# Optimization experiments

Hardware: AMD Instinct MI355X
Metric: run time of the kernel (lower is better)

Reference implementation:

```python
import jax, jax.numpy as jnp
import numpy as np

STRICT_MAXIMA_BONUS = 10.0  # init kwarg strict_maxima_bonus


def _pad_rep(x):
    # replicate-pad spatial dims (D,H,W) by 1, matching kornia F.pad(..., 'replicate')
    return jnp.pad(x, ((0, 0), (0, 0), (1, 1), (1, 1), (1, 1)), mode='edge')


def _grad1(x):
    # kornia spatial_gradient3d(order=1, mode='diff'): central differences /2
    p = _pad_rep(x)
    c, l, r = slice(1, -1), slice(0, -2), slice(2, None)
    dx = 0.5 * (p[..., c, c, r] - p[..., c, c, l])  # d/dx along W
    dy = 0.5 * (p[..., c, r, c] - p[..., c, l, c])  # d/dy along H
    ds = 0.5 * (p[..., r, c, c] - p[..., l, c, c])  # d/ds along D
    return jnp.stack([dx, dy, ds], axis=-1)  # (B,C,D,H,W,3)


def _grad2(x):
    # kornia spatial_gradient3d(order=2, mode='diff'): channel order dxx,dyy,dss,dxy,dys,dxs
    p = _pad_rep(x)
    c, l, r = slice(1, -1), slice(0, -2), slice(2, None)
    dxx = p[..., c, c, l] + p[..., c, c, r] - 2.0 * x
    dyy = p[..., c, l, c] + p[..., c, r, c] - 2.0 * x
    dss = p[..., l, c, c] + p[..., r, c, c] - 2.0 * x
    dxy = p[..., c, l, l] + p[..., c, r, r] - p[..., c, r, l] - p[..., c, l, r]
    dys = p[..., l, l, c] + p[..., r, r, c] - p[..., r, l, c] - p[..., l, r, c]
    dxs = p[..., l, c, l] + p[..., r, c, r] - p[..., r, c, l] - p[..., l, c, r]
    return dxx, dyy, dss, dxy, dys, dxs


def _nms3d_mask(x):
    # kornia nms3d: x == maxpool3d(x, 3, stride 1, pad 1) (pad value -inf)
    mx = jax.lax.reduce_window(x, -jnp.inf, jax.lax.max,
                               (1, 1, 3, 3, 3), (1, 1, 1, 1, 1),
                               [(0, 0), (0, 0), (1, 1), (1, 1), (1, 1)])
    return x == mx


def _forward(x):
    B, C, D, H, W = x.shape
    b = _grad1(x)  # (B,C,D,H,W,3) order [dx,dy,ds]
    dxx, dyy, dss, dxy, dys, dxs = _grad2(x)
    dxy, dys, dxs = 0.25 * dxy, 0.25 * dys, 0.25 * dxs
    Hes = jnp.stack([dxx, dxy, dxs,
                     dxy, dyy, dys,
                     dxs, dys, dss], axis=-1).reshape(B, C, D, H, W, 3, 3)
    nms = _nms3d_mask(x)  # (B,C,D,H,W) bool
    # safe_solve_with_mask: LU solve valid where factorization succeeded (non-singular)
    det = jnp.linalg.det(Hes)
    solved = det != 0.0
    eye3 = jnp.eye(3, dtype=x.dtype)
    safe_H = jnp.where(solved[..., None, None], Hes, eye3)
    sol = jnp.linalg.solve(safe_H, b[..., None])[..., 0]  # (B,C,D,H,W,3)
    new_nms = nms & solved  # nms_mask.masked_scatter(nms_mask, solved_correctly)
    x_solved = jnp.where(new_nms[..., None], sol, 0.0)
    dx = -x_solved
    # zero refinements with any |component| > 0.7
    big = jnp.max(jnp.abs(dx), axis=-1, keepdims=True) > 0.7
    dx = jnp.where(big, 0.0, dx)
    dy_val = 0.5 * jnp.sum(b * dx, axis=-1)  # 0.5 * b^T dx per voxel
    y_max = x + dy_val + STRICT_MAXIMA_BONUS * new_nms.astype(x.dtype)
    # dx.flip(1): component order [s,y,x]; then move comps to axis 2 -> (B,C,3,D,H,W)
    dx_res = jnp.moveaxis(dx[..., ::-1], -1, 2)
    # kornia create_meshgrid3d(...).permute(0,4,1,2,3): channel values (d, w, h)
    dd, hh, ww = jnp.meshgrid(jnp.arange(D), jnp.arange(H), jnp.arange(W), indexing='ij')
    grid = jnp.stack([dd, ww, hh], axis=0).astype(x.dtype)  # (3,D,H,W)
    coords_max = grid[None, None] + dx_res  # (B,C,3,D,H,W)
    return coords_max, y_max


def setup_inputs() -> dict:
    key = jax.random.key(0)
    x = jax.random.normal(key, (2, 1, 8, 512, 512), dtype=jnp.float32)
    return {"x": x}


def reference(x):
    return _forward(x)
```

## Files before the change

kernel.cpp:

```cpp
#include <hip/hip_runtime.h>

namespace {

constexpr int Dd = 8, Hh = 512, Ww = 512, Bb = 2;
constexpr int PLANE = Hh * Ww;
constexpr size_t COORDS_SZ = (size_t)Bb * 3 * Dd * PLANE;

__global__ __launch_bounds__(256) void cqi_kernel(const float* __restrict__ x,
                                                  float* __restrict__ out) {
    const int tx = threadIdx.x;
    const int ty = threadIdx.y;
    const int w0 = tx << 2;
    const int h  = (blockIdx.y << 1) + ty;
    const int bd = blockIdx.z;
    const int b  = bd >> 3;
    const int d  = bd & 7;

    const float* pls[3];
    pls[0] = x + (size_t)(d > 0      ? bd - 1 : bd) * PLANE;
    pls[1] = x + (size_t)bd * PLANE;
    pls[2] = x + (size_t)(d < Dd - 1 ? bd + 1 : bd) * PLANE;

    const int rws[3] = { (h > 0      ? h - 1 : 0)      * Ww,
                          h * Ww,
                         (h < Hh - 1 ? h + 1 : h)      * Ww };

    const int wm = (w0 > 0)        ? w0 - 1 : 0;
    const int wp = (w0 + 4 < Ww)   ? w0 + 4 : Ww - 1;

    float r[3][3][6];
#pragma unroll
    for (int a = 0; a < 3; ++a) {
#pragma unroll
        for (int e = 0; e < 3; ++e) {
            const float* p = pls[a] + rws[e];
            const float4 q = *reinterpret_cast<const float4*>(p + w0);
            r[a][e][0] = p[wm];
            r[a][e][1] = q.x; r[a][e][2] = q.y; r[a][e][3] = q.z; r[a][e][4] = q.w;
            r[a][e][5] = p[wp];
        }
    }

    float oc0[4], oc1[4], oc2[4], oy[4];
#pragma unroll
    for (int i = 0; i < 4; ++i) {
        float v[3][3][3];
#pragma unroll
        for (int a = 0; a < 3; ++a)
#pragma unroll
            for (int e = 0; e < 3; ++e)
#pragma unroll
                for (int cc = 0; cc < 3; ++cc)
                    v[a][e][cc] = r[a][e][i + cc];

        const float c0 = v[1][1][1];

        const float fx = 0.5f * (v[1][1][2] - v[1][1][0]);
        const float fy = 0.5f * (v[1][2][1] - v[1][0][1]);
        const float fs = 0.5f * (v[2][1][1] - v[0][1][1]);

        const float dxx = v[1][1][0] + v[1][1][2] - 2.0f * c0;
        const float dyy = v[1][0][1] + v[1][2][1] - 2.0f * c0;
        const float dss = v[0][1][1] + v[2][1][1] - 2.0f * c0;
        const float dxy = 0.25f * (v[1][0][0] + v[1][2][2] - v[1][2][0] - v[1][0][2]);
        const float dys = 0.25f * (v[0][0][1] + v[2][2][1] - v[2][0][1] - v[0][2][1]);
        const float dxs = 0.25f * (v[0][1][0] + v[2][1][2] - v[2][1][0] - v[0][1][2]);

        float mx = v[0][0][0];
#pragma unroll
        for (int a = 0; a < 3; ++a)
#pragma unroll
            for (int e = 0; e < 3; ++e)
#pragma unroll
                for (int cc = 0; cc < 3; ++cc)
                    mx = fmaxf(mx, v[a][e][cc]);
        const bool nms = (c0 == mx);

        const float det = dxx * dyy * dss + dxy * dys * dxs + dxs * dxy * dys
                        - dxs * dyy * dxs - dxx * dys * dys - dxy * dxy * dss;
        const bool solved = (det != 0.0f);

        const float A00 = dyy * dss - dys * dys;
        const float A01 = dys * dxs - dxy * dss;
        const float A02 = dxy * dys - dyy * dxs;
        const float A11 = dxx * dss - dxs * dxs;
        const float A12 = dxy * dxs - dxx * dys;
        const float A22 = dxx * dyy - dxy * dxy;
        const float inv = 1.0f / det;
        const float sx = (A00 * fx + A01 * fy + A02 * fs) * inv;
        const float sy = (A01 * fx + A11 * fy + A12 * fs) * inv;
        const float ss = (A02 * fx + A12 * fy + A22 * fs) * inv;

        const bool newnms = nms && solved;
        float dxv = newnms ? -sx : 0.0f;
        float dyv = newnms ? -sy : 0.0f;
        float dsv = newnms ? -ss : 0.0f;

        const float mabs = fmaxf(fabsf(dxv), fmaxf(fabsf(dyv), fabsf(dsv)));
        const bool keep = (mabs <= 0.7f);
        dxv = keep ? dxv : 0.0f;
        dyv = keep ? dyv : 0.0f;
        dsv = keep ? dsv : 0.0f;

        const float dyval = 0.5f * (fx * dxv + fy * dyv + fs * dsv);

        oy[i]  = c0 + dyval + (newnms ? 10.0f : 0.0f);
        oc0[i] = (float)d + dsv;
        oc1[i] = (float)(w0 + i) + dyv;
        oc2[i] = (float)h + dxv;
    }

    float* coords = out;
    float* ymax   = out + COORDS_SZ;
    const size_t idx = (size_t)(h * Ww) + w0;
    const size_t cb  = ((size_t)(b * 3) * Dd + d) * PLANE + idx;
    *reinterpret_cast<float4*>(coords + cb)                          = make_float4(oc0[0], oc0[1], oc0[2], oc0[3]);
    *reinterpret_cast<float4*>(coords + cb + (size_t)Dd * PLANE)     = make_float4(oc1[0], oc1[1], oc1[2], oc1[3]);
    *reinterpret_cast<float4*>(coords + cb + (size_t)2 * Dd * PLANE) = make_float4(oc2[0], oc2[1], oc2[2], oc2[3]);
    *reinterpret_cast<float4*>(ymax + (size_t)bd * PLANE + idx)      = make_float4(oy[0], oy[1], oy[2], oy[3]);
}

}

extern "C" void kernel_launch(void* const* d_in, const int* in_sizes, int n_in,
                              void* d_out, int out_size, void* d_ws, size_t ws_size,
                              hipStream_t stream) {
    const float* x = (const float*)d_in[0];
    float* out = (float*)d_out;
    dim3 grid(1, Hh / 2, Bb * Dd);
    dim3 block(Ww / 4, 2, 1);
    hipLaunchKernelGGL(cqi_kernel, grid, block, 0, stream, x, out);
}
```

Before: 96.60 us.

## Process eight voxels per thread with one wavefront per row and shuffle halos

Each 64-lane wavefront now covers one full 512-wide row, and each thread handles eight consecutive voxels loaded as two float4s. The left and right halo values come from neighbouring lanes via cross-lane shuffles instead of extra scalar global loads. The aim is to remove the redundant halo loads and amortize per-thread setup over more outputs. The cost is higher register pressure from the 3x3x10 window, plus a new dependency on a 64-wide wavefront.

New measurement: 92.20 us. -4.5%, faster.

```diff
diff --git a/kernel.cpp b/kernel.cpp
--- a/kernel.cpp
+++ b/kernel.cpp
@@ -8,116 +8,116 @@
 
 __global__ __launch_bounds__(256) void cqi_kernel(const float* __restrict__ x,
                                                   float* __restrict__ out) {
-    const int tx = threadIdx.x;
-    const int ty = threadIdx.y;
-    const int w0 = tx << 2;
-    const int h  = (blockIdx.y << 1) + ty;
-    const int bd = blockIdx.z;
+    const int lane = threadIdx.x & 63;
+    const int gid  = (blockIdx.x << 2) | (threadIdx.x >> 6);
+    const int h  = gid & (Hh - 1);
+    const int bd = gid >> 9;
     const int b  = bd >> 3;
     const int d  = bd & 7;
 
-    const float* pls[3];
-    pls[0] = x + (size_t)(d > 0      ? bd - 1 : bd) * PLANE;
-    pls[1] = x + (size_t)bd * PLANE;
-    pls[2] = x + (size_t)(d < Dd - 1 ? bd + 1 : bd) * PLANE;
+    const float* pl[3];
+    pl[0] = x + (size_t)(d > 0      ? bd - 1 : bd) * PLANE;
+    pl[1] = x + (size_t)bd * PLANE;
+    pl[2] = x + (size_t)(d < Dd - 1 ? bd + 1 : bd) * PLANE;
+    const int rw[3] = { (h > 0      ? h - 1 : 0) * Ww,
+                         h * Ww,
+                        (h < Hh - 1 ? h + 1 : h) * Ww };
 
-    const int rws[3] = { (h > 0      ? h - 1 : 0)      * Ww,
-                          h * Ww,
-                         (h < Hh - 1 ? h + 1 : h)      * Ww };
+    const int w0 = lane << 3;
 
-    const int wm = (w0 > 0)        ? w0 - 1 : 0;
-    const int wp = (w0 + 4 < Ww)   ? w0 + 4 : Ww - 1;
-
-    float r[3][3][6];
+    float W[3][3][10];
 #pragma unroll
     for (int a = 0; a < 3; ++a) {
 #pragma unroll
         for (int e = 0; e < 3; ++e) {
-            const float* p = pls[a] + rws[e];
-            const float4 q = *reinterpret_cast<const float4*>(p + w0);
-            r[a][e][0] = p[wm];
-            r[a][e][1] = q.x; r[a][e][2] = q.y; r[a][e][3] = q.z; r[a][e][4] = q.w;
-            r[a][e][5] = p[wp];
+            const float* p = pl[a] + rw[e] + w0;
+            const float4 q0 = *reinterpret_cast<const float4*>(p);
+            const float4 q1 = *reinterpret_cast<const float4*>(p + 4);
+            const float lh = __shfl_up(q1.w, 1);
+            const float rh = __shfl_down(q0.x, 1);
+            W[a][e][0] = (lane == 0)  ? q0.x : lh;
+            W[a][e][1] = q0.x; W[a][e][2] = q0.y; W[a][e][3] = q0.z; W[a][e][4] = q0.w;
+            W[a][e][5] = q1.x; W[a][e][6] = q1.y; W[a][e][7] = q1.z; W[a][e][8] = q1.w;
+            W[a][e][9] = (lane == 63) ? q1.w : rh;
         }
-    }
-
-    float oc0[4], oc1[4], oc2[4], oy[4];
-#pragma unroll
-    for (int i = 0; i < 4; ++i) {
-        float v[3][3][3];
-#pragma unroll
-        for (int a = 0; a < 3; ++a)
-#pragma unroll
-            for (int e = 0; e < 3; ++e)
-#pragma unroll
-                for (int cc = 0; cc < 3; ++cc)
-                    v[a][e][cc] = r[a][e][i + cc];
-
-        const float c0 = v[1][1][1];
-
-        const float fx = 0.5f * (v[1][1][2] - v[1][1][0]);
-        const float fy = 0.5f * (v[1][2][1] - v[1][0][1]);
-        const float fs = 0.5f * (v[2][1][1] - v[0][1][1]);
-
-        const float dxx = v[1][1][0] + v[1][1][2] - 2.0f * c0;
-        const float dyy = v[1][0][1] + v[1][2][1] - 2.0f * c0;
-        const float dss = v[0][1][1] + v[2][1][1] - 2.0f * c0;
-        const float dxy = 0.25f * (v[1][0][0] + v[1][2][2] - v[1][2][0] - v[1][0][2]);
-        const float dys = 0.25f * (v[0][0][1] + v[2][2][1] - v[2][0][1] - v[0][2][1]);
-        const float dxs = 0.25f * (v[0][1][0] + v[2][1][2] - v[2][1][0] - v[0][1][2]);
-
-        float mx = v[0][0][0];
-#pragma unroll
-        for (int a = 0; a < 3; ++a)
-#pragma unroll
-            for (int e = 0; e < 3; ++e)
-#pragma unroll
-                for (int cc = 0; cc < 3; ++cc)
-                    mx = fmaxf(mx, v[a][e][cc]);
-        const bool nms = (c0 == mx);
-
-        const float det = dxx * dyy * dss + dxy * dys * dxs + dxs * dxy * dys
-                        - dxs * dyy * dxs - dxx * dys * dys - dxy * dxy * dss;
-        const bool solved = (det != 0.0f);
-
-        const float A00 = dyy * dss - dys * dys;
-        const float A01 = dys * dxs - dxy * dss;
-        const float A02 = dxy * dys - dyy * dxs;
-        const float A11 = dxx * dss - dxs * dxs;
-        const float A12 = dxy * dxs - dxx * dys;
-        const float A22 = dxx * dyy - dxy * dxy;
-        const float inv = 1.0f / det;
-        const float sx = (A00 * fx + A01 * fy + A02 * fs) * inv;
-        const float sy = (A01 * fx + A11 * fy + A12 * fs) * inv;
-        const float ss = (A02 * fx + A12 * fy + A22 * fs) * inv;
-
-        const bool newnms = nms && solved;
-        float dxv = newnms ? -sx : 0.0f;
-        float dyv = newnms ? -sy : 0.0f;
-        float dsv = newnms ? -ss : 0.0f;
-
-        const float mabs = fmaxf(fabsf(dxv), fmaxf(fabsf(dyv), fabsf(dsv)));
-        const bool keep = (mabs <= 0.7f);
-        dxv = keep ? dxv : 0.0f;
-        dyv = keep ? dyv : 0.0f;
-        dsv = keep ? dsv : 0.0f;
-
-        const float dyval = 0.5f * (fx * dxv + fy * dyv + fs * dsv);
-
-        oy[i]  = c0 + dyval + (newnms ? 10.0f : 0.0f);
-        oc0[i] = (float)d + dsv;
-        oc1[i] = (float)(w0 + i) + dyv;
-        oc2[i] = (float)h + dxv;
     }
 
     float* coords = out;
     float* ymax   = out + COORDS_SZ;
     const size_t idx = (size_t)(h * Ww) + w0;
     const size_t cb  = ((size_t)(b * 3) * Dd + d) * PLANE + idx;
-    *reinterpret_cast<float4*>(coords + cb)                          = make_float4(oc0[0], oc0[1], oc0[2], oc0[3]);
-    *reinterpret_cast<float4*>(coords + cb + (size_t)Dd * PLANE)     = make_float4(oc1[0], oc1[1], oc1[2], oc1[3]);
-    *reinterpret_cast<float4*>(coords + cb + (size_t)2 * Dd * PLANE) = make_float4(oc2[0], oc2[1], oc2[2], oc2[3]);
-    *reinterpret_cast<float4*>(ymax + (size_t)bd * PLANE + idx)      = make_float4(oy[0], oy[1], oy[2], oy[3]);
+    const size_t yb  = (size_t)bd * PLANE + idx;
+
+#pragma unroll
+    for (int half = 0; half < 2; ++half) {
+        float4 oc0, oc1, oc2, oy;
+        float* oc0p = &oc0.x; float* oc1p = &oc1.x;
+        float* oc2p = &oc2.x; float* oyp = &oy.x;
+#pragma unroll
+        for (int j = 0; j < 4; ++j) {
+            const int i = half * 4 + j;
+            const float c0 = W[1][1][i + 1];
+
+            const float fx = 0.5f * (W[1][1][i + 2] - W[1][1][i]);
+            const float fy = 0.5f * (W[1][2][i + 1] - W[1][0][i + 1]);
+            const float fs = 0.5f * (W[2][1][i + 1] - W[0][1][i + 1]);
+
+            const float dxx = W[1][1][i] + W[1][1][i + 2] - 2.0f * c0;
+            const float dyy = W[1][0][i + 1] + W[1][2][i + 1] - 2.0f * c0;
+            const float dss = W[0][1][i + 1] + W[2][1][i + 1] - 2.0f * c0;
+            const float dxy = 0.25f * (W[1][0][i] + W[1][2][i + 2] - W[1][2][i] - W[1][0][i + 2]);
+            const float dys = 0.25f * (W[0][0][i + 1] + W[2][2][i + 1] - W[2][0][i + 1] - W[0][2][i + 1]);
+            const float dxs = 0.25f * (W[0][1][i] + W[2][1][i + 2] - W[2][1][i] - W[0][1][i + 2]);
+
+            float mx = W[0][0][i];
+#pragma unroll
+            for (int a = 0; a < 3; ++a)
+#pragma unroll
+                for (int e = 0; e < 3; ++e)
+#pragma unroll
+                    for (int cc = 0; cc < 3; ++cc)
+                        mx = fmaxf(mx, W[a][e][i + cc]);
+            const bool nms = (c0 == mx);
+
+            const float det = dxx * dyy * dss + dxy * dys * dxs + dxs * dxy * dys
+                            - dxs * dyy * dxs - dxx * dys * dys - dxy * dxy * dss;
+            const bool solved = (det != 0.0f);
+
+            const float A00 = dyy * dss - dys * dys;
+            const float A01 = dys * dxs - dxy * dss;
+            const float A02 = dxy * dys - dyy * dxs;
+            const float A11 = dxx * dss - dxs * dxs;
+            const float A12 = dxy * dxs - dxx * dys;
+            const float A22 = dxx * dyy - dxy * dxy;
+            const float inv = 1.0f / det;
+            const float sx = (A00 * fx + A01 * fy + A02 * fs) * inv;
+            const float sy = (A01 * fx + A11 * fy + A12 * fs) * inv;
+            const float ss = (A02 * fx + A12 * fy + A22 * fs) * inv;
+
+            const bool newnms = nms && solved;
+            float dxv = newnms ? -sx : 0.0f;
+            float dyv = newnms ? -sy : 0.0f;
+            float dsv = newnms ? -ss : 0.0f;
+
+            const float mabs = fmaxf(fabsf(dxv), fmaxf(fabsf(dyv), fabsf(dsv)));
+            const bool keep = (mabs <= 0.7f);
+            dxv = keep ? dxv : 0.0f;
+            dyv = keep ? dyv : 0.0f;
+            dsv = keep ? dsv : 0.0f;
+
+            const float dyval = 0.5f * (fx * dxv + fy * dyv + fs * dsv);
+
+            oyp[j]  = c0 + dyval + (newnms ? 10.0f : 0.0f);
+            oc0p[j] = (float)d + dsv;
+            oc1p[j] = (float)(w0 + i) + dyv;
+            oc2p[j] = (float)h + dxv;
+        }
+        const size_t off = (size_t)(half * 4);
+        *reinterpret_cast<float4*>(coords + cb + off)                          = oc0;
+        *reinterpret_cast<float4*>(coords + cb + (size_t)Dd * PLANE + off)     = oc1;
+        *reinterpret_cast<float4*>(coords + cb + (size_t)2 * Dd * PLANE + off) = oc2;
+        *reinterpret_cast<float4*>(ymax + yb + off)                            = oy;
+    }
 }
 
 }
@@ -127,7 +127,7 @@
                               hipStream_t stream) {
     const float* x = (const float*)d_in[0];
     float* out = (float*)d_out;
-    dim3 grid(1, Hh / 2, Bb * Dd);
-    dim3 block(Ww / 4, 2, 1);
+    dim3 grid(Bb * Dd * Hh / 4, 1, 1);
+    dim3 block(256, 1, 1);
     hipLaunchKernelGGL(cqi_kernel, grid, block, 0, stream, x, out);
 }
```
